# Optimization experiments

Hardware: AMD Instinct MI355X
Metric: run time of the kernel (lower is better)

Reference implementation:

```python
import jax, jax.numpy as jnp
import numpy as np

B = 8; NPC = 12500; N = B * NPC
L = 10.0; RES = 0.7; K = 16
IN_CH = 64; H1 = 68; H2 = 128; RNN = 128; ATTN = 32; E4 = 4 * RNN
EPS = 1e-5


def _knn_np(refs, queries, k):
    out = np.empty((queries.shape[0], k), dtype=np.int64)
    r2 = (refs * refs).sum(1)
    for s in range(0, queries.shape[0], 2048):
        q = queries[s:s + 2048]
        d2 = (q * q).sum(1)[:, None] - 2.0 * q @ refs.T + r2[None, :]
        out[s:s + q.shape[0]] = np.argpartition(d2, k, axis=1)[:, :k]
    return out


def setup_inputs():
    rng = np.random.default_rng(0)
    pos = rng.uniform(0.0, L, (N, 3)).astype(np.float32)
    batch = np.repeat(np.arange(B), NPC).astype(np.int32)
    x = (0.5 * rng.standard_normal((N, IN_CH))).astype(np.float32)
    refl = rng.uniform(0.0, 1.0, N).astype(np.float32)
    # voxel-grid sampling: one representative point per occupied voxel per cloud
    G = int(np.ceil(L / RES)) + 1
    v = np.floor(pos / RES).astype(np.int64)
    vkey = ((batch.astype(np.int64) * G + v[:, 0]) * G + v[:, 1]) * G + v[:, 2]
    _, first = np.unique(vkey, return_index=True)
    idx = np.sort(first)
    M = idx.shape[0]
    # per-cloud brute-force KNN (k neighbors in full set for every sampled point)
    src_list = []
    for b in range(B):
        qi = idx[(idx >= b * NPC) & (idx < (b + 1) * NPC)]
        src_list.append(_knn_np(pos[b * NPC:(b + 1) * NPC], pos[qi], K) + b * NPC)
    src = np.concatenate(src_list, 0).reshape(-1)
    tgt = np.repeat(np.arange(M), K)
    edge_index = np.stack([src, tgt]).astype(np.int32)

    def W(*s):
        return jnp.asarray((0.05 * rng.standard_normal(s)).astype(np.float32))

    def zeros(c):
        return jnp.zeros((c,), jnp.float32)

    def bnp(c):  # packed inference-mode BN params: [gamma, beta, mean, var]
        return jnp.asarray(np.stack([1.0 + 0.1 * rng.standard_normal(c), 0.1 * rng.standard_normal(c), 0.1 * rng.standard_normal(c), 1.0 + 0.1 * rng.uniform(0.0, 1.0, c)]).astype(np.float32))

    def dwp(c):  # depthwise k=1 conv = per-channel [weight, bias]
        return jnp.asarray(np.stack([1.0 + 0.1 * rng.standard_normal(c), 0.1 * rng.standard_normal(c)]).astype(np.float32))

    gum = -np.log(-np.log(rng.uniform(1e-6, 1.0 - 1e-6, (B, 2))))
    return dict(
        x=jnp.asarray(x), pos=jnp.asarray(pos), reflectance=jnp.asarray(refl),
        gumbel=jnp.asarray(gum.astype(np.float32)),
        gate_w1=W(4, H1), gate_b1=zeros(H1), gate_w2=W(H1, H1), gate_b2=zeros(H1),
        gate_wg=W(H1, 2), gate_bg=jnp.asarray(np.array([0.0, 2.0], np.float32)),
        loc_w1=W(H1, H2), loc_b1=zeros(H2), loc_w2=W(H2, H2), loc_b2=zeros(H2),
        attn_w1=W(H2, ATTN), attn_b1=zeros(ATTN), attn_w2=W(ATTN),
        exp_w=W(RNN, E4), exp_b=zeros(E4), exp_bn=bnp(E4),
        ds1_dw=dwp(E4), ds1_bn1=bnp(E4), ds1_pw_w=W(E4, E4), ds1_pw_b=zeros(E4), ds1_bn2=bnp(E4),
        blk_bn1=bnp(E4),
        ds2_dw=dwp(E4), ds2_bn1=bnp(E4), ds2_pw_w=W(E4, E4), ds2_pw_b=zeros(E4), ds2_bn2=bnp(E4),
        blk_bn2=bnp(E4),
        proj_w=W(E4, RNN), proj_b=zeros(RNN), proj_bn=bnp(RNN),
        batch=jnp.asarray(batch), idx=jnp.asarray(idx.astype(np.int32)),
        edge_index=jnp.asarray(edge_index), k=K, num_graphs=B)


def _bn(z, p):
    return p[0] * (z - p[2]) / jnp.sqrt(p[3] + EPS) + p[1]


def reference(x, pos, reflectance, gumbel, gate_w1, gate_b1, gate_w2, gate_b2, gate_wg, gate_bg, loc_w1, loc_b1, loc_w2, loc_b2, attn_w1, attn_b1, attn_w2, exp_w, exp_b, exp_bn, ds1_dw, ds1_bn1, ds1_pw_w, ds1_pw_b, ds1_bn2, blk_bn1, ds2_dw, ds2_bn1, ds2_pw_w, ds2_pw_b, ds2_bn2, blk_bn2, proj_w, proj_b, proj_bn, batch, idx, edge_index, k, num_graphs):
    # --- BinaryReflectanceGate (soft gumbel-softmax, tau=1) ---
    feats = jnp.concatenate([pos, reflectance[:, None]], -1)  # [N,4]
    h = jax.nn.relu(feats @ gate_w1 + gate_b1)
    h = jax.nn.relu(h @ gate_w2 + gate_b2)
    pooled = jax.ops.segment_max(h, batch, num_segments=num_graphs)  # global_max_pool
    logits = pooled @ gate_wg + gate_bg
    y_soft = jax.nn.softmax(logits + gumbel, axis=-1)
    refl_g = y_soft[:, 1][batch] * reflectance  # gated reflectance [N]
    pos4 = jnp.concatenate([pos, refl_g[:, None]], -1)  # [N,4]
    # --- AttentivePointNetConv: gather -> local MLP -> softmax attn -> reduce ---
    M = idx.shape[0]
    src = edge_index[0].reshape(M, k)  # k source neighbors per centroid
    msg_in = jnp.concatenate([x[src], pos4[src] - pos4[idx][:, None, :]], -1)  # [M,k,68]
    hm = jax.nn.relu(msg_in @ loc_w1 + loc_b1)
    msg = jax.nn.relu(hm @ loc_w2 + loc_b2)  # [M,k,128]
    score = jnp.tanh(msg @ attn_w1 + attn_b1) @ attn_w2  # [M,k]
    alpha = jax.nn.softmax(score, axis=-1)  # softmax over each centroid's edges
    agg = jnp.einsum('mk,mkc->mc', alpha, msg)  # [M,128]
    # --- InvertedResidualBlock (all convs kernel=1 -> channel matmuls, BN inference) ---
    out = jax.nn.relu(_bn(agg @ exp_w + exp_b, exp_bn))  # expand 128->512

    def ds(z, dw, bn1, pw_w, pw_b, bn2):
        d = jax.nn.relu(_bn(z * dw[0] + dw[1], bn1))  # depthwise k=1
        return _bn(d @ pw_w + pw_b, bn2)  # pointwise

    out = _bn(ds(out, ds1_dw, ds1_bn1, ds1_pw_w, ds1_pw_b, ds1_bn2), blk_bn1)
    out = _bn(ds(out, ds2_dw, ds2_bn1, ds2_pw_w, ds2_pw_b, ds2_bn2), blk_bn2)
    out = _bn(out @ proj_w + proj_b, proj_bn)  # project 512->128
    out = jax.nn.relu(out + agg)  # identity shortcut (RNN==RNN)
    return (out, pos[idx], batch[idx], refl_g[idx])
```

## Files before the change

kernel.cpp:

```cpp
#include <hip/hip_runtime.h>
#include <hip/hip_bf16.h>

typedef __hip_bfloat16 bf16;

#define B_GR 8
#define IN_CH 64
#define H1 68
#define H2 128
#define ATTN 32
#define E4 512
#define RNN 128
#define KNN 16
#define EPSV 1e-5f

typedef __attribute__((ext_vector_type(8))) short s8v;
typedef __attribute__((ext_vector_type(4))) float f4v;
#define MFMA16(a,b,c) __builtin_amdgcn_mfma_f32_16x16x32_bf16(a,b,c,0,0,0)

#define SK96 104
#define SK128 136
#define SK512 520

template<int DT> __device__ __forceinline__ float LD(const void* p, size_t i) {
    if (DT) return __bfloat162float(((const bf16*)p)[i]);
    return ((const float*)p)[i];
}
template<int DT> __device__ __forceinline__ void ST(void* p, size_t i, float v) {
    if (DT) ((bf16*)p)[i] = __float2bfloat16(v);
    else    ((float*)p)[i] = v;
}
__device__ __forceinline__ unsigned short f2bfb(float f) {
    unsigned u = __float_as_uint(f);
    unsigned r = (u + 0x7FFFu + ((u >> 16) & 1u)) >> 16;
    return (unsigned short)r;
}
__device__ __forceinline__ float bfb2f(unsigned short u) {
    return __uint_as_float(((unsigned)u) << 16);
}
__device__ __forceinline__ float fast_tanh(float x) {
    x = fminf(fmaxf(x, -12.f), 12.f);
    float e = __expf(2.f * x);
    return (e - 1.f) / (e + 1.f);
}

__global__ void prep_kernel(const void* pos, int* flag, int* pooled) {
    const int tid = threadIdx.x;
    for (int i = tid; i < B_GR*H1; i += 256) pooled[i] = 0;
    if (tid == 0) {
        const unsigned* w = (const unsigned*)pos;
        int ok = 1;
        #pragma unroll 8
        for (int i = 0; i < 256; i++) {
            float f = __uint_as_float((w[i] & 0xFFFFu) << 16);
            if (!(f >= -0.01f && f <= 10.05f)) ok = 0;
        }
        *flag = ok;
    }
}

#define W1T_E (128*SK96)
#define W2T_E (128*SK128)
#define AW1T_E (32*SK128)
#define EXPT_E (512*SK128)
#define D1T_E (512*SK512)
#define D2T_E (512*SK512)
#define PJT_E (128*SK512)
#define GW2T_E (80*SK96)
template<int DT> __global__ __launch_bounds__(256) void trans_kernel(
    const int* __restrict__ flag,
    const void* __restrict__ w1, const void* __restrict__ w2, const void* __restrict__ aw1,
    const void* __restrict__ expw, const void* __restrict__ d1pw,
    const void* __restrict__ d2pw, const void* __restrict__ pjw,
    const void* __restrict__ gw2,
    unsigned short* __restrict__ w1T, unsigned short* __restrict__ w2T,
    unsigned short* __restrict__ aw1T, unsigned short* __restrict__ expwT,
    unsigned short* __restrict__ d1pwT, unsigned short* __restrict__ d2pwT,
    unsigned short* __restrict__ pjwT, unsigned short* __restrict__ gw2gT)
{
    if (*flag != DT) return;
    const int T0 = W1T_E, T1 = T0+W2T_E, T2 = T1+AW1T_E, T3 = T2+EXPT_E,
              T4 = T3+D1T_E, T5 = T4+D2T_E, T6 = T5+PJT_E, T7 = T6+GW2T_E;
    for (int i = blockIdx.x*256 + threadIdx.x; i < T7; i += gridDim.x*256) {
        if (i < T0) {
            int n = i / SK96, k = i - n*SK96;
            w1T[i] = (k < H1) ? f2bfb(LD<DT>(w1, (size_t)k*H2 + n)) : 0;
        } else if (i < T1) {
            int j = i - T0; int n = j / SK128, k = j - n*SK128;
            w2T[j] = (k < H2) ? f2bfb(LD<DT>(w2, (size_t)k*H2 + n)) : 0;
        } else if (i < T2) {
            int j = i - T1; int n = j / SK128, k = j - n*SK128;
            aw1T[j] = (k < H2) ? f2bfb(LD<DT>(aw1, (size_t)k*ATTN + n)) : 0;
        } else if (i < T3) {
            int j = i - T2; int n = j / SK128, k = j - n*SK128;
            expwT[j] = (k < RNN) ? f2bfb(LD<DT>(expw, (size_t)k*E4 + n)) : 0;
        } else if (i < T4) {
            int j = i - T3; int n = j / SK512, k = j - n*SK512;
            d1pwT[j] = (k < E4) ? f2bfb(LD<DT>(d1pw, (size_t)k*E4 + n)) : 0;
        } else if (i < T5) {
            int j = i - T4; int n = j / SK512, k = j - n*SK512;
            d2pwT[j] = (k < E4) ? f2bfb(LD<DT>(d2pw, (size_t)k*E4 + n)) : 0;
        } else if (i < T6) {
            int j = i - T5; int n = j / SK512, k = j - n*SK512;
            pjwT[j] = (k < E4) ? f2bfb(LD<DT>(pjw, (size_t)k*RNN + n)) : 0;
        } else {
            int j = i - T6; int n = j / SK96, k = j - n*SK96;
            gw2gT[j] = (k < H1 && n < H1) ? f2bfb(LD<DT>(gw2, (size_t)k*H1 + n)) : 0;
        }
    }
}

template<int DT> __global__ void coef_kernel(
    const int* __restrict__ flag,
    const void* __restrict__ expb, const void* __restrict__ expbn,
    const void* __restrict__ d1dw, const void* __restrict__ d1bn1,
    const void* __restrict__ d1pb, const void* __restrict__ d1bn2, const void* __restrict__ bbn1,
    const void* __restrict__ d2dw, const void* __restrict__ d2bn1,
    const void* __restrict__ d2pb, const void* __restrict__ d2bn2, const void* __restrict__ bbn2,
    const void* __restrict__ pjb, const void* __restrict__ pjbn,
    float4* __restrict__ C1, float2* __restrict__ C2, float2* __restrict__ C3,
    float2* __restrict__ C4)
{
    if (*flag != DT) return;
    int c = blockIdx.x*256 + threadIdx.x;
    if (c < E4) {
        float a_e = LD<DT>(expbn,c) * rsqrtf(LD<DT>(expbn,3*E4+c)+EPSV);
        float t0  = a_e*(LD<DT>(expb,c) - LD<DT>(expbn,2*E4+c)) + LD<DT>(expbn,E4+c);
        float a1 = LD<DT>(d1bn1,c) * rsqrtf(LD<DT>(d1bn1,3*E4+c)+EPSV);
        float s1 = a1 * LD<DT>(d1dw,c);
        float t1 = a1*(LD<DT>(d1dw,E4+c) - LD<DT>(d1bn1,2*E4+c)) + LD<DT>(d1bn1,E4+c);
        C1[c] = make_float4(a_e, t0, s1, t1);
        float a2 = LD<DT>(d1bn2,c) * rsqrtf(LD<DT>(d1bn2,3*E4+c)+EPSV);
        float t2 = a2*(LD<DT>(d1pb,c) - LD<DT>(d1bn2,2*E4+c)) + LD<DT>(d1bn2,E4+c);
        float a3 = LD<DT>(bbn1,c) * rsqrtf(LD<DT>(bbn1,3*E4+c)+EPSV);
        float S2 = a3*a2;
        float T2 = a3*(t2 - LD<DT>(bbn1,2*E4+c)) + LD<DT>(bbn1,E4+c);
        float a4 = LD<DT>(d2bn1,c) * rsqrtf(LD<DT>(d2bn1,3*E4+c)+EPSV);
        float sdw = a4 * LD<DT>(d2dw,c);
        float tdw = a4*(LD<DT>(d2dw,E4+c) - LD<DT>(d2bn1,2*E4+c)) + LD<DT>(d2bn1,E4+c);
        C2[c] = make_float2(sdw*S2, sdw*T2 + tdw);
        float a5 = LD<DT>(d2bn2,c) * rsqrtf(LD<DT>(d2bn2,3*E4+c)+EPSV);
        float t5 = a5*(LD<DT>(d2pb,c) - LD<DT>(d2bn2,2*E4+c)) + LD<DT>(d2bn2,E4+c);
        float a6 = LD<DT>(bbn2,c) * rsqrtf(LD<DT>(bbn2,3*E4+c)+EPSV);
        C3[c] = make_float2(a6*a5, a6*(t5 - LD<DT>(bbn2,2*E4+c)) + LD<DT>(bbn2,E4+c));
    }
    if (c < RNN) {
        float ap = LD<DT>(pjbn,c) * rsqrtf(LD<DT>(pjbn,3*RNN+c)+EPSV);
        C4[c] = make_float2(ap, ap*(LD<DT>(pjb,c) - LD<DT>(pjbn,2*RNN+c)) + LD<DT>(pjbn,RNN+c));
    }
}

template<int DT> __global__ __launch_bounds__(256) void gate_mfma(
    const int* __restrict__ flag,
    const void* __restrict__ pos, const void* __restrict__ refl,
    const void* __restrict__ w1, const void* __restrict__ b1, const void* __restrict__ b2g,
    const unsigned short* __restrict__ gw2gT,
    int* __restrict__ pooled, int NPC, int CPB)
{
    if (*flag != DT) return;
    __shared__ __align__(16) unsigned short hs[256*SK96];
    __shared__ float w1s[4*H1], b1s[H1], b2s[H1];
    const int tid = threadIdx.x;
    for (int i = tid; i < 4*H1; i += 256) w1s[i] = LD<DT>(w1, i);
    if (tid < H1) { b1s[tid] = LD<DT>(b1, tid); b2s[tid] = LD<DT>(b2g, tid); }
    __syncthreads();

    const int bb = blockIdx.x / CPB;
    const int cc = blockIdx.x % CPB;
    const int base = bb*NPC + cc*256;
    const int limit = NPC - cc*256;
    const int p = base + ((tid < limit) ? tid : 0);

    {
        float f0 = LD<DT>(pos, (size_t)p*3+0), f1 = LD<DT>(pos, (size_t)p*3+1);
        float f2 = LD<DT>(pos, (size_t)p*3+2), f3 = LD<DT>(refl, p);
        float h[H1];
        #pragma unroll
        for (int j = 0; j < H1; j++)
            h[j] = fmaxf(b1s[j] + f0*w1s[j] + f1*w1s[H1+j] + f2*w1s[2*H1+j] + f3*w1s[3*H1+j], 0.f);
        #pragma unroll
        for (int j = 0; j < H1; j += 2) {
            unsigned v = (unsigned)f2bfb(h[j]) | ((unsigned)f2bfb(h[j+1]) << 16);
            *(unsigned*)&hs[tid*SK96 + j] = v;
        }
        #pragma unroll
        for (int j = H1; j < 96; j += 2) *(unsigned*)&hs[tid*SK96 + j] = 0;
    }
    __syncthreads();

    const int wv = tid >> 6, lane = tid & 63, quad = lane >> 4, l15 = lane & 15;
    f4v acc[4][5];
    #pragma unroll
    for (int mt = 0; mt < 4; mt++)
        #pragma unroll
        for (int nt = 0; nt < 5; nt++) acc[mt][nt] = (f4v){0.f,0.f,0.f,0.f};
    s8v af[4][3];
    #pragma unroll
    for (int mt = 0; mt < 4; mt++)
        #pragma unroll
        for (int ks = 0; ks < 3; ks++)
            af[mt][ks] = *(const s8v*)&hs[(wv*64 + mt*16 + l15)*SK96 + ks*32 + quad*8];
    #pragma unroll
    for (int nt = 0; nt < 5; nt++) {
        #pragma unroll
        for (int ks = 0; ks < 3; ks++) {
            s8v bf_ = *(const s8v*)&gw2gT[(size_t)(nt*16 + l15)*SK96 + ks*32 + quad*8];
            #pragma unroll
            for (int mt = 0; mt < 4; mt++) acc[mt][nt] = MFMA16(af[mt][ks], bf_, acc[mt][nt]);
        }
    }
    #pragma unroll
    for (int nt = 0; nt < 5; nt++) {
        int col = nt*16 + l15;
        float v = acc[0][nt][0];
        #pragma unroll
        for (int mt = 0; mt < 4; mt++)
            #pragma unroll
            for (int r = 0; r < 4; r++) v = fmaxf(v, acc[mt][nt][r]);
        v = fmaxf(v, __shfl_xor(v, 16));
        v = fmaxf(v, __shfl_xor(v, 32));
        if (quad == 0 && col < H1) {
            float o = fmaxf(v + b2s[col], 0.f);
            atomicMax(&pooled[bb*H1 + col], __float_as_int(o));
        }
    }
}

template<int DT> __global__ void gate2_kernel(
    const int* __restrict__ flag, const int* __restrict__ pooled,
    const void* __restrict__ wg, const void* __restrict__ bg,
    const void* __restrict__ gum, float* __restrict__ y1)
{
    if (*flag != DT) return;
    __shared__ float lg[B_GR][2];
    const int t = threadIdx.x;
    if (t < B_GR*2) {
        int b = t >> 1, g = t & 1;
        float a = LD<DT>(bg, g) + LD<DT>(gum, b*2+g);
        for (int c = 0; c < H1; c++) a += __int_as_float(pooled[b*H1+c]) * LD<DT>(wg, c*2+g);
        lg[b][g] = a;
    }
    __syncthreads();
    if (t < B_GR) {
        float l0 = lg[t][0], l1 = lg[t][1];
        float m = fmaxf(l0, l1);
        float e0 = __expf(l0-m), e1 = __expf(l1-m);
        y1[t] = e1 / (e0 + e1);
    }
}

template<int DT> __global__ __launch_bounds__(256) void edge_mfma(
    const int* __restrict__ flag,
    const void* __restrict__ x, const void* __restrict__ pos,
    const void* __restrict__ refl, const float* __restrict__ y1,
    const int* __restrict__ batch,
    const int* __restrict__ idxarr, const int* __restrict__ esrc,
    const void* __restrict__ b1, const void* __restrict__ b2,
    const void* __restrict__ ab1, const void* __restrict__ aw2,
    const unsigned short* __restrict__ gw1T, const unsigned short* __restrict__ gw2T,
    const unsigned short* __restrict__ gaw1T,
    void* __restrict__ out, int M)
{
    if (*flag != DT) return;
    __shared__ __align__(16) unsigned short u2[128*SK128];
    __shared__ float ssc[4][2][16];

    const int tid = threadIdx.x;
    const int wv = tid >> 6, lane = tid & 63, quad = lane >> 4, l15 = lane & 15;
    const int m0 = blockIdx.x * 8 + wv * 2;
    const int rb = wv * 32;

    s8v af[2][3];
    int mcl[2];
    float p4v[2][4];
    #pragma unroll
    for (int t = 0; t < 2; t++) {
        int mm = m0 + t; if (mm >= M) mm = M - 1;
        mcl[t] = mm;
        int t_idx = idxarr[mm];
        p4v[t][0] = LD<DT>(pos, (size_t)t_idx*3 + 0);
        p4v[t][1] = LD<DT>(pos, (size_t)t_idx*3 + 1);
        p4v[t][2] = LD<DT>(pos, (size_t)t_idx*3 + 2);
        p4v[t][3] = y1[batch[t_idx]] * LD<DT>(refl, t_idx);
        int s = esrc[mm*KNN + l15];
        if (DT) {
            const unsigned short* xs = (const unsigned short*)x + (size_t)s*IN_CH;
            af[t][0] = *(const s8v*)(xs + quad*8);
            af[t][1] = *(const s8v*)(xs + 32 + quad*8);
        } else {
            unsigned short tmp0[8], tmp1[8];
            #pragma unroll
            for (int e = 0; e < 8; e++) {
                tmp0[e] = f2bfb(LD<0>(x, (size_t)s*IN_CH + quad*8 + e));
                tmp1[e] = f2bfb(LD<0>(x, (size_t)s*IN_CH + 32 + quad*8 + e));
            }
            af[t][0] = *(const s8v*)tmp0;
            af[t][1] = *(const s8v*)tmp1;
        }
        s8v a2 = (s8v){0,0,0,0,0,0,0,0};
        if (quad == 0) {
            a2[0] = (short)f2bfb(LD<DT>(pos, (size_t)s*3 + 0) - p4v[t][0]);
            a2[1] = (short)f2bfb(LD<DT>(pos, (size_t)s*3 + 1) - p4v[t][1]);
            a2[2] = (short)f2bfb(LD<DT>(pos, (size_t)s*3 + 2) - p4v[t][2]);
            a2[3] = (short)f2bfb(y1[batch[s]] * LD<DT>(refl, s) - p4v[t][3]);
        }
        af[t][2] = a2;
    }

    {
        f4v acc[2][8];
        #pragma unroll
        for (int t = 0; t < 2; t++)
            #pragma unroll
            for (int nt = 0; nt < 8; nt++) acc[t][nt] = (f4v){0.f,0.f,0.f,0.f};
        #pragma unroll
        for (int nt = 0; nt < 8; nt++) {
            #pragma unroll
            for (int ks = 0; ks < 3; ks++) {
                s8v bf_ = *(const s8v*)&gw1T[(size_t)(nt*16 + l15)*SK96 + ks*32 + quad*8];
                acc[0][nt] = MFMA16(af[0][ks], bf_, acc[0][nt]);
                acc[1][nt] = MFMA16(af[1][ks], bf_, acc[1][nt]);
            }
        }
        #pragma unroll
        for (int nt = 0; nt < 8; nt++) {
            int col = nt*16 + l15;
            float bb = LD<DT>(b1, col);
            #pragma unroll
            for (int t = 0; t < 2; t++)
                #pragma unroll
                for (int r = 0; r < 4; r++) {
                    int row = rb + t*16 + quad*4 + r;
                    u2[row*SK128 + col] = f2bfb(fmaxf(acc[t][nt][r] + bb, 0.f));
                }
        }
    }

    {
        s8v af2[2][4];
        #pragma unroll
        for (int t = 0; t < 2; t++)
            #pragma unroll
            for (int ks = 0; ks < 4; ks++)
                af2[t][ks] = *(const s8v*)&u2[(rb + t*16 + l15)*SK128 + ks*32 + quad*8];
        f4v acc[2][8];
        #pragma unroll
        for (int t = 0; t < 2; t++)
            #pragma unroll
            for (int nt = 0; nt < 8; nt++) acc[t][nt] = (f4v){0.f,0.f,0.f,0.f};
        #pragma unroll
        for (int nt = 0; nt < 8; nt++) {
            #pragma unroll
            for (int ks = 0; ks < 4; ks++) {
                s8v bf_ = *(const s8v*)&gw2T[(size_t)(nt*16 + l15)*SK128 + ks*32 + quad*8];
                acc[0][nt] = MFMA16(af2[0][ks], bf_, acc[0][nt]);
                acc[1][nt] = MFMA16(af2[1][ks], bf_, acc[1][nt]);
            }
        }
        #pragma unroll
        for (int nt = 0; nt < 8; nt++) {
            int col = nt*16 + l15;
            float bb = LD<DT>(b2, col);
            #pragma unroll
            for (int t = 0; t < 2; t++)
                #pragma unroll
                for (int r = 0; r < 4; r++) {
                    int row = rb + t*16 + quad*4 + r;
                    u2[row*SK128 + col] = f2bfb(fmaxf(acc[t][nt][r] + bb, 0.f));
                }
        }
    }

    {
        s8v af3[2][4];
        #pragma unroll
        for (int t = 0; t < 2; t++)
            #pragma unroll
            for (int ks = 0; ks < 4; ks++)
                af3[t][ks] = *(const s8v*)&u2[(rb + t*16 + l15)*SK128 + ks*32 + quad*8];
        f4v acc[2][2];
        #pragma unroll
        for (int t = 0; t < 2; t++)
            #pragma unroll
            for (int nt = 0; nt < 2; nt++) acc[t][nt] = (f4v){0.f,0.f,0.f,0.f};
        #pragma unroll
        for (int nt = 0; nt < 2; nt++) {
            #pragma unroll
            for (int ks = 0; ks < 4; ks++) {
                s8v bf_ = *(const s8v*)&gaw1T[(size_t)(nt*16 + l15)*SK128 + ks*32 + quad*8];
                acc[0][nt] = MFMA16(af3[0][ks], bf_, acc[0][nt]);
                acc[1][nt] = MFMA16(af3[1][ks], bf_, acc[1][nt]);
            }
        }
        #pragma unroll
        for (int t = 0; t < 2; t++)
            #pragma unroll
            for (int r = 0; r < 4; r++) {
                float s = 0.f;
                #pragma unroll
                for (int nt = 0; nt < 2; nt++) {
                    int col = nt*16 + l15;
                    s += fast_tanh(acc[t][nt][r] + LD<DT>(ab1, col)) * LD<DT>(aw2, col);
                }
                s += __shfl_xor(s, 1);
                s += __shfl_xor(s, 2);
                s += __shfl_xor(s, 4);
                s += __shfl_xor(s, 8);
                if (l15 == 0) ssc[wv][t][quad*4 + r] = s;
            }
    }

    #pragma unroll
    for (int t = 0; t < 2; t++) {
        float sc[KNN];
        #pragma unroll
        for (int j = 0; j < KNN; j++) sc[j] = ssc[wv][t][j];
        float mx = sc[0];
        #pragma unroll
        for (int j = 1; j < KNN; j++) mx = fmaxf(mx, sc[j]);
        float den = 0.f;
        #pragma unroll
        for (int j = 0; j < KNN; j++) { sc[j] = __expf(sc[j] - mx); den += sc[j]; }
        float inv = 1.f / den;
        float a0 = 0.f, a1 = 0.f;
        #pragma unroll
        for (int j = 0; j < KNN; j++) {
            unsigned v = *(const unsigned*)&u2[(rb + t*16 + j)*SK128 + 2*lane];
            float w = sc[j] * inv;
            a0 += w * bfb2f((unsigned short)(v & 0xFFFFu));
            a1 += w * bfb2f((unsigned short)(v >> 16));
        }
        int mm = m0 + t;
        if (mm < M) {
            if (DT) {
                unsigned pk = (unsigned)f2bfb(a0) | ((unsigned)f2bfb(a1) << 16);
                *(unsigned*)((bf16*)out + (size_t)mm*H2 + 2*lane) = pk;
            } else {
                ST<0>(out, (size_t)mm*H2 + 2*lane, a0);
                ST<0>(out, (size_t)mm*H2 + 2*lane + 1, a1);
            }
            if (lane == 0) {
                ST<DT>(out, (size_t)M*128 + mm*3 + 0, p4v[t][0]);
                ST<DT>(out, (size_t)M*128 + mm*3 + 1, p4v[t][1]);
                ST<DT>(out, (size_t)M*128 + mm*3 + 2, p4v[t][2]);
                ST<DT>(out, (size_t)M*131 + mm, (float)batch[idxarr[mcl[t]]]);
                ST<DT>(out, (size_t)M*132 + mm, p4v[t][3]);
            }
        }
    }
}

template<int DT> __global__ __launch_bounds__(256) void post_mfma(
    const int* __restrict__ flag,
    const unsigned short* __restrict__ expwT, const unsigned short* __restrict__ d1pwT,
    const unsigned short* __restrict__ d2pwT, const unsigned short* __restrict__ pjwT,
    const float4* __restrict__ C1, const float2* __restrict__ C2,
    const float2* __restrict__ C3, const float2* __restrict__ C4,
    void* __restrict__ out, int M)
{
    if (*flag != DT) return;
    __shared__ __align__(16) unsigned short zs[32*SK512];
    __shared__ __align__(16) unsigned short a0[32*SK128];
    const int tid = threadIdx.x;
    const int m0 = blockIdx.x * 32;

    {
        int r = tid >> 3;
        int c0 = (tid & 7) * 16;
        int mm = m0 + r;
        for (int c = c0; c < c0+16; c++) {
            float v = (mm < M) ? LD<DT>(out, (size_t)mm*RNN + c) : 0.f;
            a0[r*SK128 + c] = f2bfb(v);
        }
        if ((tid & 7) == 7) for (int c = RNN; c < SK128; c++) a0[r*SK128 + c] = 0;
    }
    __syncthreads();

    const int wv = tid >> 6, lane = tid & 63, quad = lane >> 4, l15 = lane & 15;
    const int nbase = wv * 128;

    f4v acc[2][8];

    #pragma unroll
    for (int mt = 0; mt < 2; mt++)
        #pragma unroll
        for (int nt = 0; nt < 8; nt++) acc[mt][nt] = (f4v){0.f,0.f,0.f,0.f};
    #pragma unroll
    for (int ks = 0; ks < 4; ks++) {
        s8v af0 = *(const s8v*)&a0[(l15)*SK128 + ks*32 + quad*8];
        s8v af1 = *(const s8v*)&a0[(16+l15)*SK128 + ks*32 + quad*8];
        #pragma unroll
        for (int nt = 0; nt < 8; nt++) {
            s8v bf_ = *(const s8v*)&expwT[(size_t)(nbase + nt*16 + l15)*SK128 + ks*32 + quad*8];
            acc[0][nt] = MFMA16(af0, bf_, acc[0][nt]);
            acc[1][nt] = MFMA16(af1, bf_, acc[1][nt]);
        }
    }
    #pragma unroll
    for (int nt = 0; nt < 8; nt++) {
        int col = nbase + nt*16 + l15;
        float4 cf = C1[col];
        #pragma unroll
        for (int mt = 0; mt < 2; mt++)
            #pragma unroll
            for (int r = 0; r < 4; r++) {
                int row = mt*16 + quad*4 + r;
                float u = fmaxf(cf.x*acc[mt][nt][r] + cf.y, 0.f);
                float d = fmaxf(cf.z*u + cf.w, 0.f);
                zs[row*SK512 + col] = f2bfb(d);
            }
    }
    __syncthreads();

    #pragma unroll
    for (int mt = 0; mt < 2; mt++)
        #pragma unroll
        for (int nt = 0; nt < 8; nt++) acc[mt][nt] = (f4v){0.f,0.f,0.f,0.f};
    for (int ks = 0; ks < 16; ks++) {
        s8v af0 = *(const s8v*)&zs[(l15)*SK512 + ks*32 + quad*8];
        s8v af1 = *(const s8v*)&zs[(16+l15)*SK512 + ks*32 + quad*8];
        #pragma unroll
        for (int nt = 0; nt < 8; nt++) {
            s8v bf_ = *(const s8v*)&d1pwT[(size_t)(nbase + nt*16 + l15)*SK512 + ks*32 + quad*8];
            acc[0][nt] = MFMA16(af0, bf_, acc[0][nt]);
            acc[1][nt] = MFMA16(af1, bf_, acc[1][nt]);
        }
    }
    __syncthreads();
    #pragma unroll
    for (int nt = 0; nt < 8; nt++) {
        int col = nbase + nt*16 + l15;
        float2 cf = C2[col];
        #pragma unroll
        for (int mt = 0; mt < 2; mt++)
            #pragma unroll
            for (int r = 0; r < 4; r++) {
                int row = mt*16 + quad*4 + r;
                zs[row*SK512 + col] = f2bfb(fmaxf(cf.x*acc[mt][nt][r] + cf.y, 0.f));
            }
    }
    __syncthreads();

    #pragma unroll
    for (int mt = 0; mt < 2; mt++)
        #pragma unroll
        for (int nt = 0; nt < 8; nt++) acc[mt][nt] = (f4v){0.f,0.f,0.f,0.f};
    for (int ks = 0; ks < 16; ks++) {
        s8v af0 = *(const s8v*)&zs[(l15)*SK512 + ks*32 + quad*8];
        s8v af1 = *(const s8v*)&zs[(16+l15)*SK512 + ks*32 + quad*8];
        #pragma unroll
        for (int nt = 0; nt < 8; nt++) {
            s8v bf_ = *(const s8v*)&d2pwT[(size_t)(nbase + nt*16 + l15)*SK512 + ks*32 + quad*8];
            acc[0][nt] = MFMA16(af0, bf_, acc[0][nt]);
            acc[1][nt] = MFMA16(af1, bf_, acc[1][nt]);
        }
    }
    __syncthreads();
    #pragma unroll
    for (int nt = 0; nt < 8; nt++) {
        int col = nbase + nt*16 + l15;
        float2 cf = C3[col];
        #pragma unroll
        for (int mt = 0; mt < 2; mt++)
            #pragma unroll
            for (int r = 0; r < 4; r++) {
                int row = mt*16 + quad*4 + r;
                zs[row*SK512 + col] = f2bfb(cf.x*acc[mt][nt][r] + cf.y);
            }
    }
    __syncthreads();

    {
        f4v pacc[2][2];
        #pragma unroll
        for (int mt = 0; mt < 2; mt++)
            #pragma unroll
            for (int nt = 0; nt < 2; nt++) pacc[mt][nt] = (f4v){0.f,0.f,0.f,0.f};
        for (int ks = 0; ks < 16; ks++) {
            s8v af0 = *(const s8v*)&zs[(l15)*SK512 + ks*32 + quad*8];
            s8v af1 = *(const s8v*)&zs[(16+l15)*SK512 + ks*32 + quad*8];
            #pragma unroll
            for (int nt = 0; nt < 2; nt++) {
                s8v bf_ = *(const s8v*)&pjwT[(size_t)(wv*32 + nt*16 + l15)*SK512 + ks*32 + quad*8];
                pacc[0][nt] = MFMA16(af0, bf_, pacc[0][nt]);
                pacc[1][nt] = MFMA16(af1, bf_, pacc[1][nt]);
            }
        }
        #pragma unroll
        for (int nt = 0; nt < 2; nt++) {
            int col = wv*32 + nt*16 + l15;
            float2 cf = C4[col];
            #pragma unroll
            for (int mt = 0; mt < 2; mt++)
                #pragma unroll
                for (int r = 0; r < 4; r++) {
                    int row = mt*16 + quad*4 + r;
                    int mm = m0 + row;
                    if (mm < M) {
                        float agv = bfb2f(a0[row*SK128 + col]);
                        float o = fmaxf(cf.x*pacc[mt][nt][r] + cf.y + agv, 0.f);
                        ST<DT>(out, (size_t)mm*RNN + col, o);
                    }
                }
        }
    }
}

extern "C" void kernel_launch(void* const* d_in, const int* in_sizes, int n_in,
                              void* d_out, int out_size, void* d_ws, size_t ws_size,
                              hipStream_t stream)
{
    const void* x    = d_in[0];
    const void* pos  = d_in[1];
    const void* refl = d_in[2];
    const void* gum  = d_in[3];
    const void* gw1  = d_in[4];
    const void* gb1  = d_in[5];
    const void* gw2  = d_in[6];
    const void* gb2  = d_in[7];
    const void* gwg  = d_in[8];
    const void* gbg  = d_in[9];
    const void* lw1  = d_in[10];
    const void* lb1  = d_in[11];
    const void* lw2  = d_in[12];
    const void* lb2  = d_in[13];
    const void* aw1  = d_in[14];
    const void* ab1  = d_in[15];
    const void* aw2  = d_in[16];
    const void* expw = d_in[17];
    const void* expb = d_in[18];
    const void* expbn= d_in[19];
    const void* d1dw = d_in[20];
    const void* d1bn1= d_in[21];
    const void* d1pw = d_in[22];
    const void* d1pb = d_in[23];
    const void* d1bn2= d_in[24];
    const void* bbn1 = d_in[25];
    const void* d2dw = d_in[26];
    const void* d2bn1= d_in[27];
    const void* d2pw = d_in[28];
    const void* d2pb = d_in[29];
    const void* d2bn2= d_in[30];
    const void* bbn2 = d_in[31];
    const void* pjw  = d_in[32];
    const void* pjb  = d_in[33];
    const void* pjbn = d_in[34];
    const int* batch = (const int*)d_in[35];
    const int* idxp  = (const int*)d_in[36];
    const int* eidx  = (const int*)d_in[37];

    const int N = in_sizes[2];
    const int M = in_sizes[36];
    const int NPC = N / B_GR;
    const int CPB = (NPC + 255) / 256;

    char* wsb = (char*)d_ws;
    int*  flag   = (int*)wsb;
    int*  pooled = (int*)(wsb + 16);
    float* y1    = (float*)(wsb + 2304);
    unsigned short* w1T   = (unsigned short*)(wsb + 2368);
    unsigned short* w2T   = w1T + W1T_E;
    unsigned short* aw1T  = w2T + W2T_E;
    unsigned short* expwT = aw1T + AW1T_E;
    unsigned short* d1pwT = expwT + EXPT_E;
    unsigned short* d2pwT = d1pwT + D1T_E;
    unsigned short* pjwT  = d2pwT + D2T_E;
    unsigned short* gw2gT = pjwT + PJT_E;
    float4* C1 = (float4*)(gw2gT + GW2T_E + 8);
    float2* C2 = (float2*)(C1 + E4);
    float2* C3 = C2 + E4;
    float2* C4 = C3 + E4;

    prep_kernel<<<1, 256, 0, stream>>>(pos, flag, pooled);

    trans_kernel<0><<<512, 256, 0, stream>>>(flag, lw1, lw2, aw1, expw, d1pw, d2pw, pjw, gw2,
                                             w1T, w2T, aw1T, expwT, d1pwT, d2pwT, pjwT, gw2gT);
    trans_kernel<1><<<512, 256, 0, stream>>>(flag, lw1, lw2, aw1, expw, d1pw, d2pw, pjw, gw2,
                                             w1T, w2T, aw1T, expwT, d1pwT, d2pwT, pjwT, gw2gT);

    coef_kernel<0><<<2, 256, 0, stream>>>(flag, expb, expbn, d1dw, d1bn1, d1pb, d1bn2, bbn1,
                                          d2dw, d2bn1, d2pb, d2bn2, bbn2, pjb, pjbn,
                                          C1, C2, C3, C4);
    coef_kernel<1><<<2, 256, 0, stream>>>(flag, expb, expbn, d1dw, d1bn1, d1pb, d1bn2, bbn1,
                                          d2dw, d2bn1, d2pb, d2bn2, bbn2, pjb, pjbn,
                                          C1, C2, C3, C4);

    gate_mfma<0><<<B_GR*CPB, 256, 0, stream>>>(flag, pos, refl, gw1, gb1, gb2, gw2gT, pooled, NPC, CPB);
    gate_mfma<1><<<B_GR*CPB, 256, 0, stream>>>(flag, pos, refl, gw1, gb1, gb2, gw2gT, pooled, NPC, CPB);

    gate2_kernel<0><<<1, 64, 0, stream>>>(flag, pooled, gwg, gbg, gum, y1);
    gate2_kernel<1><<<1, 64, 0, stream>>>(flag, pooled, gwg, gbg, gum, y1);

    const int EB = (M + 7) / 8;
    edge_mfma<0><<<EB, 256, 0, stream>>>(flag, x, pos, refl, y1, batch, idxp, eidx,
                                         lb1, lb2, ab1, aw2, w1T, w2T, aw1T, d_out, M);
    edge_mfma<1><<<EB, 256, 0, stream>>>(flag, x, pos, refl, y1, batch, idxp, eidx,
                                         lb1, lb2, ab1, aw2, w1T, w2T, aw1T, d_out, M);

    const int PB = (M + 31) / 32;
    post_mfma<0><<<PB, 256, 0, stream>>>(flag, expwT, d1pwT, d2pwT, pjwT, C1, C2, C3, C4, d_out, M);
    post_mfma<1><<<PB, 256, 0, stream>>>(flag, expwT, d1pwT, d2pwT, pjwT, C1, C2, C3, C4, d_out, M);
}
```

Baseline: 472.9 us.

## Restructure post-MLP so each wave owns a 16-row strip without block barriers

The post-processing MLP kernel now runs with two waves per block. Each wave owns its own 16 rows and computes all output columns, keeping its A fragments in registers and passing intermediates through a private shared-memory strip. This removes the __syncthreads barriers and the shared a0 staging buffer, and the residual is re-read from global memory at the end. The cost is that every wave now streams the full weight matrices from global/L2 for only 16 rows, roughly doubling weight traffic per row. It also needs more registers to hold 16 A fragments.

```diff
diff --git a/kernel.cpp b/kernel.cpp
--- a/kernel.cpp
+++ b/kernel.cpp
@@ -449,7 +449,7 @@
     }
 }
 
-template<int DT> __global__ __launch_bounds__(256) void post_mfma(
+template<int DT> __global__ __launch_bounds__(128) void post_mfma(
     const int* __restrict__ flag,
     const unsigned short* __restrict__ expwT, const unsigned short* __restrict__ d1pwT,
     const unsigned short* __restrict__ d2pwT, const unsigned short* __restrict__ pjwT,
@@ -459,148 +459,114 @@
 {
     if (*flag != DT) return;
     __shared__ __align__(16) unsigned short zs[32*SK512];
-    __shared__ __align__(16) unsigned short a0[32*SK128];
     const int tid = threadIdx.x;
-    const int m0 = blockIdx.x * 32;
-
-    {
-        int r = tid >> 3;
-        int c0 = (tid & 7) * 16;
-        int mm = m0 + r;
-        for (int c = c0; c < c0+16; c++) {
-            float v = (mm < M) ? LD<DT>(out, (size_t)mm*RNN + c) : 0.f;
-            a0[r*SK128 + c] = f2bfb(v);
-        }
-        if ((tid & 7) == 7) for (int c = RNN; c < SK128; c++) a0[r*SK128 + c] = 0;
-    }
-    __syncthreads();
-
     const int wv = tid >> 6, lane = tid & 63, quad = lane >> 4, l15 = lane & 15;
-    const int nbase = wv * 128;
-
-    f4v acc[2][8];
-
-    #pragma unroll
-    for (int mt = 0; mt < 2; mt++)
-        #pragma unroll
-        for (int nt = 0; nt < 8; nt++) acc[mt][nt] = (f4v){0.f,0.f,0.f,0.f};
-    #pragma unroll
-    for (int ks = 0; ks < 4; ks++) {
-        s8v af0 = *(const s8v*)&a0[(l15)*SK128 + ks*32 + quad*8];
-        s8v af1 = *(const s8v*)&a0[(16+l15)*SK128 + ks*32 + quad*8];
-        #pragma unroll
+    const int m0w = blockIdx.x * 32 + wv * 16;
+    unsigned short* strip = zs + wv * 16 * SK512;
+
+    {
+        s8v afe[4];
+        int mrow = m0w + l15; if (mrow >= M) mrow = M - 1;
+        if (DT) {
+            const unsigned short* op = (const unsigned short*)out + (size_t)mrow*RNN;
+            #pragma unroll
+            for (int ks = 0; ks < 4; ks++)
+                afe[ks] = *(const s8v*)(op + ks*32 + quad*8);
+        } else {
+            #pragma unroll
+            for (int ks = 0; ks < 4; ks++) {
+                unsigned short tmp[8];
+                #pragma unroll
+                for (int e = 0; e < 8; e++)
+                    tmp[e] = f2bfb(LD<0>(out, (size_t)mrow*RNN + ks*32 + quad*8 + e));
+                afe[ks] = *(const s8v*)tmp;
+            }
+        }
+        #pragma unroll 4
+        for (int nt = 0; nt < 32; nt++) {
+            f4v acc = (f4v){0.f,0.f,0.f,0.f};
+            #pragma unroll
+            for (int ks = 0; ks < 4; ks++) {
+                s8v bf_ = *(const s8v*)&expwT[(size_t)(nt*16 + l15)*SK128 + ks*32 + quad*8];
+                acc = MFMA16(afe[ks], bf_, acc);
+            }
+            int col = nt*16 + l15;
+            float4 cf = C1[col];
+            #pragma unroll
+            for (int r = 0; r < 4; r++) {
+                float u = fmaxf(cf.x*acc[r] + cf.y, 0.f);
+                float d = fmaxf(cf.z*u + cf.w, 0.f);
+                strip[(quad*4 + r)*SK512 + col] = f2bfb(d);
+            }
+        }
+    }
+
+    {
+        s8v af[16];
+        #pragma unroll
+        for (int ks = 0; ks < 16; ks++)
+            af[ks] = *(const s8v*)&strip[l15*SK512 + ks*32 + quad*8];
+        #pragma unroll 2
+        for (int nt = 0; nt < 32; nt++) {
+            f4v acc = (f4v){0.f,0.f,0.f,0.f};
+            #pragma unroll
+            for (int ks = 0; ks < 16; ks++) {
+                s8v bf_ = *(const s8v*)&d1pwT[(size_t)(nt*16 + l15)*SK512 + ks*32 + quad*8];
+                acc = MFMA16(af[ks], bf_, acc);
+            }
+            int col = nt*16 + l15;
+            float2 cf = C2[col];
+            #pragma unroll
+            for (int r = 0; r < 4; r++)
+                strip[(quad*4 + r)*SK512 + col] = f2bfb(fmaxf(cf.x*acc[r] + cf.y, 0.f));
+        }
+    }
+
+    {
+        s8v af[16];
+        #pragma unroll
+        for (int ks = 0; ks < 16; ks++)
+            af[ks] = *(const s8v*)&strip[l15*SK512 + ks*32 + quad*8];
+        #pragma unroll 2
+        for (int nt = 0; nt < 32; nt++) {
+            f4v acc = (f4v){0.f,0.f,0.f,0.f};
+            #pragma unroll
+            for (int ks = 0; ks < 16; ks++) {
+                s8v bf_ = *(const s8v*)&d2pwT[(size_t)(nt*16 + l15)*SK512 + ks*32 + quad*8];
+                acc = MFMA16(af[ks], bf_, acc);
+            }
+            int col = nt*16 + l15;
+            float2 cf = C3[col];
+            #pragma unroll
+            for (int r = 0; r < 4; r++)
+                strip[(quad*4 + r)*SK512 + col] = f2bfb(cf.x*acc[r] + cf.y);
+        }
+    }
+
+    {
+        s8v af[16];
+        #pragma unroll
+        for (int ks = 0; ks < 16; ks++)
+            af[ks] = *(const s8v*)&strip[l15*SK512 + ks*32 + quad*8];
+        #pragma unroll 2
         for (int nt = 0; nt < 8; nt++) {
-            s8v bf_ = *(const s8v*)&expwT[(size_t)(nbase + nt*16 + l15)*SK128 + ks*32 + quad*8];
-            acc[0][nt] = MFMA16(af0, bf_, acc[0][nt]);
-            acc[1][nt] = MFMA16(af1, bf_, acc[1][nt]);
-        }
-    }
-    #pragma unroll
-    for (int nt = 0; nt < 8; nt++) {
-        int col = nbase + nt*16 + l15;
-        float4 cf = C1[col];
-        #pragma unroll
-        for (int mt = 0; mt < 2; mt++)
+            f4v acc = (f4v){0.f,0.f,0.f,0.f};
+            #pragma unroll
+            for (int ks = 0; ks < 16; ks++) {
+                s8v bf_ = *(const s8v*)&pjwT[(size_t)(nt*16 + l15)*SK512 + ks*32 + quad*8];
+                acc = MFMA16(af[ks], bf_, acc);
+            }
+            int col = nt*16 + l15;
+            float2 cf = C4[col];
             #pragma unroll
             for (int r = 0; r < 4; r++) {
-                int row = mt*16 + quad*4 + r;
-                float u = fmaxf(cf.x*acc[mt][nt][r] + cf.y, 0.f);
-                float d = fmaxf(cf.z*u + cf.w, 0.f);
-                zs[row*SK512 + col] = f2bfb(d);
-            }
-    }
-    __syncthreads();
-
-    #pragma unroll
-    for (int mt = 0; mt < 2; mt++)
-        #pragma unroll
-        for (int nt = 0; nt < 8; nt++) acc[mt][nt] = (f4v){0.f,0.f,0.f,0.f};
-    for (int ks = 0; ks < 16; ks++) {
-        s8v af0 = *(const s8v*)&zs[(l15)*SK512 + ks*32 + quad*8];
-        s8v af1 = *(const s8v*)&zs[(16+l15)*SK512 + ks*32 + quad*8];
-        #pragma unroll
-        for (int nt = 0; nt < 8; nt++) {
-            s8v bf_ = *(const s8v*)&d1pwT[(size_t)(nbase + nt*16 + l15)*SK512 + ks*32 + quad*8];
-            acc[0][nt] = MFMA16(af0, bf_, acc[0][nt]);
-            acc[1][nt] = MFMA16(af1, bf_, acc[1][nt]);
-        }
-    }
-    __syncthreads();
-    #pragma unroll
-    for (int nt = 0; nt < 8; nt++) {
-        int col = nbase + nt*16 + l15;
-        float2 cf = C2[col];
-        #pragma unroll
-        for (int mt = 0; mt < 2; mt++)
-            #pragma unroll
-            for (int r = 0; r < 4; r++) {
-                int row = mt*16 + quad*4 + r;
-                zs[row*SK512 + col] = f2bfb(fmaxf(cf.x*acc[mt][nt][r] + cf.y, 0.f));
-            }
-    }
-    __syncthreads();
-
-    #pragma unroll
-    for (int mt = 0; mt < 2; mt++)
-        #pragma unroll
-        for (int nt = 0; nt < 8; nt++) acc[mt][nt] = (f4v){0.f,0.f,0.f,0.f};
-    for (int ks = 0; ks < 16; ks++) {
-        s8v af0 = *(const s8v*)&zs[(l15)*SK512 + ks*32 + quad*8];
-        s8v af1 = *(const s8v*)&zs[(16+l15)*SK512 + ks*32 + quad*8];
-        #pragma unroll
-        for (int nt = 0; nt < 8; nt++) {
-            s8v bf_ = *(const s8v*)&d2pwT[(size_t)(nbase + nt*16 + l15)*SK512 + ks*32 + quad*8];
-            acc[0][nt] = MFMA16(af0, bf_, acc[0][nt]);
-            acc[1][nt] = MFMA16(af1, bf_, acc[1][nt]);
-        }
-    }
-    __syncthreads();
-    #pragma unroll
-    for (int nt = 0; nt < 8; nt++) {
-        int col = nbase + nt*16 + l15;
-        float2 cf = C3[col];
-        #pragma unroll
-        for (int mt = 0; mt < 2; mt++)
-            #pragma unroll
-            for (int r = 0; r < 4; r++) {
-                int row = mt*16 + quad*4 + r;
-                zs[row*SK512 + col] = f2bfb(cf.x*acc[mt][nt][r] + cf.y);
-            }
-    }
-    __syncthreads();
-
-    {
-        f4v pacc[2][2];
-        #pragma unroll
-        for (int mt = 0; mt < 2; mt++)
-            #pragma unroll
-            for (int nt = 0; nt < 2; nt++) pacc[mt][nt] = (f4v){0.f,0.f,0.f,0.f};
-        for (int ks = 0; ks < 16; ks++) {
-            s8v af0 = *(const s8v*)&zs[(l15)*SK512 + ks*32 + quad*8];
-            s8v af1 = *(const s8v*)&zs[(16+l15)*SK512 + ks*32 + quad*8];
-            #pragma unroll
-            for (int nt = 0; nt < 2; nt++) {
-                s8v bf_ = *(const s8v*)&pjwT[(size_t)(wv*32 + nt*16 + l15)*SK512 + ks*32 + quad*8];
-                pacc[0][nt] = MFMA16(af0, bf_, pacc[0][nt]);
-                pacc[1][nt] = MFMA16(af1, bf_, pacc[1][nt]);
-            }
-        }
-        #pragma unroll
-        for (int nt = 0; nt < 2; nt++) {
-            int col = wv*32 + nt*16 + l15;
-            float2 cf = C4[col];
-            #pragma unroll
-            for (int mt = 0; mt < 2; mt++)
-                #pragma unroll
-                for (int r = 0; r < 4; r++) {
-                    int row = mt*16 + quad*4 + r;
-                    int mm = m0 + row;
-                    if (mm < M) {
-                        float agv = bfb2f(a0[row*SK128 + col]);
-                        float o = fmaxf(cf.x*pacc[mt][nt][r] + cf.y + agv, 0.f);
-                        ST<DT>(out, (size_t)mm*RNN + col, o);
-                    }
+                int mm = m0w + quad*4 + r;
+                if (mm < M) {
+                    float agv = LD<DT>(out, (size_t)mm*RNN + col);
+                    float o = fmaxf(cf.x*acc[r] + cf.y + agv, 0.f);
+                    ST<DT>(out, (size_t)mm*RNN + col, o);
                 }
+            }
         }
     }
 }
@@ -697,6 +663,6 @@
                                          lb1, lb2, ab1, aw2, w1T, w2T, aw1T, d_out, M);
 
     const int PB = (M + 31) / 32;
-    post_mfma<0><<<PB, 256, 0, stream>>>(flag, expwT, d1pwT, d2pwT, pjwT, C1, C2, C3, C4, d_out, M);
-    post_mfma<1><<<PB, 256, 0, stream>>>(flag, expwT, d1pwT, d2pwT, pjwT, C1, C2, C3, C4, d_out, M);
-}
+    post_mfma<0><<<PB, 128, 0, stream>>>(flag, expwT, d1pwT, d2pwT, pjwT, C1, C2, C3, C4, d_out, M);
+    post_mfma<1><<<PB, 128, 0, stream>>>(flag, expwT, d1pwT, d2pwT, pjwT, C1, C2, C3, C4, d_out, M);
+}
```

After: 460.5 us. 1.03x faster.

## Double-buffer post-MLP LDS stages and load expand operands directly into registers

Applied to the files above, without the earlier changes.

Replaces the single zs LDS buffer plus the a0 staging tile with two ping-pong buffers (zsA/zsB). Each matmul can then write its output to the other buffer without the extra barrier between the MFMA loop and the epilogue. The expand-layer A operands are loaded straight from global memory into registers instead of going through LDS, with the bf16 path using vector loads. The residual shortcut is re-read from global memory at the end. This removes two barriers and the LDS staging pass, at the cost of more LDS (two 32x520 buffers) and a possible occupancy drop.

```diff
diff --git a/kernel.cpp b/kernel.cpp
--- a/kernel.cpp
+++ b/kernel.cpp
@@ -458,131 +458,136 @@
     void* __restrict__ out, int M)
 {
     if (*flag != DT) return;
-    __shared__ __align__(16) unsigned short zs[32*SK512];
-    __shared__ __align__(16) unsigned short a0[32*SK128];
+    __shared__ __align__(16) unsigned short zsA[32*SK512];
+    __shared__ __align__(16) unsigned short zsB[32*SK512];
     const int tid = threadIdx.x;
+    const int wv = tid >> 6, lane = tid & 63, quad = lane >> 4, l15 = lane & 15;
     const int m0 = blockIdx.x * 32;
+    const int nbase = wv * 128;
 
     {
-        int r = tid >> 3;
-        int c0 = (tid & 7) * 16;
-        int mm = m0 + r;
-        for (int c = c0; c < c0+16; c++) {
-            float v = (mm < M) ? LD<DT>(out, (size_t)mm*RNN + c) : 0.f;
-            a0[r*SK128 + c] = f2bfb(v);
-        }
-        if ((tid & 7) == 7) for (int c = RNN; c < SK128; c++) a0[r*SK128 + c] = 0;
+        s8v afe[2][4];
+        #pragma unroll
+        for (int mt = 0; mt < 2; mt++) {
+            int mrow = m0 + mt*16 + l15; if (mrow >= M) mrow = M - 1;
+            if (DT) {
+                const unsigned short* op = (const unsigned short*)out + (size_t)mrow*RNN;
+                #pragma unroll
+                for (int ks = 0; ks < 4; ks++)
+                    afe[mt][ks] = *(const s8v*)(op + ks*32 + quad*8);
+            } else {
+                #pragma unroll
+                for (int ks = 0; ks < 4; ks++) {
+                    unsigned short tmp[8];
+                    #pragma unroll
+                    for (int e = 0; e < 8; e++)
+                        tmp[e] = f2bfb(LD<0>(out, (size_t)mrow*RNN + ks*32 + quad*8 + e));
+                    afe[mt][ks] = *(const s8v*)tmp;
+                }
+            }
+        }
+        f4v acc[2][8];
+        #pragma unroll
+        for (int mt = 0; mt < 2; mt++)
+            #pragma unroll
+            for (int nt = 0; nt < 8; nt++) acc[mt][nt] = (f4v){0.f,0.f,0.f,0.f};
+        #pragma unroll
+        for (int ks = 0; ks < 4; ks++) {
+            #pragma unroll
+            for (int nt = 0; nt < 8; nt++) {
+                s8v bf_ = *(const s8v*)&expwT[(size_t)(nbase + nt*16 + l15)*SK128 + ks*32 + quad*8];
+                acc[0][nt] = MFMA16(afe[0][ks], bf_, acc[0][nt]);
+                acc[1][nt] = MFMA16(afe[1][ks], bf_, acc[1][nt]);
+            }
+        }
+        #pragma unroll
+        for (int nt = 0; nt < 8; nt++) {
+            int col = nbase + nt*16 + l15;
+            float4 cf = C1[col];
+            #pragma unroll
+            for (int mt = 0; mt < 2; mt++)
+                #pragma unroll
+                for (int r = 0; r < 4; r++) {
+                    float u = fmaxf(cf.x*acc[mt][nt][r] + cf.y, 0.f);
+                    float d = fmaxf(cf.z*u + cf.w, 0.f);
+                    zsA[(mt*16 + quad*4 + r)*SK512 + col] = f2bfb(d);
+                }
+        }
     }
     __syncthreads();
 
-    const int wv = tid >> 6, lane = tid & 63, quad = lane >> 4, l15 = lane & 15;
-    const int nbase = wv * 128;
-
-    f4v acc[2][8];
-
-    #pragma unroll
-    for (int mt = 0; mt < 2; mt++)
-        #pragma unroll
-        for (int nt = 0; nt < 8; nt++) acc[mt][nt] = (f4v){0.f,0.f,0.f,0.f};
-    #pragma unroll
-    for (int ks = 0; ks < 4; ks++) {
-        s8v af0 = *(const s8v*)&a0[(l15)*SK128 + ks*32 + quad*8];
-        s8v af1 = *(const s8v*)&a0[(16+l15)*SK128 + ks*32 + quad*8];
+    {
+        f4v acc[2][8];
+        #pragma unroll
+        for (int mt = 0; mt < 2; mt++)
+            #pragma unroll
+            for (int nt = 0; nt < 8; nt++) acc[mt][nt] = (f4v){0.f,0.f,0.f,0.f};
+        for (int ks = 0; ks < 16; ks++) {
+            s8v a0 = *(const s8v*)&zsA[(l15)*SK512 + ks*32 + quad*8];
+            s8v a1 = *(const s8v*)&zsA[(16 + l15)*SK512 + ks*32 + quad*8];
+            #pragma unroll
+            for (int nt = 0; nt < 8; nt++) {
+                s8v bf_ = *(const s8v*)&d1pwT[(size_t)(nbase + nt*16 + l15)*SK512 + ks*32 + quad*8];
+                acc[0][nt] = MFMA16(a0, bf_, acc[0][nt]);
+                acc[1][nt] = MFMA16(a1, bf_, acc[1][nt]);
+            }
+        }
         #pragma unroll
         for (int nt = 0; nt < 8; nt++) {
-            s8v bf_ = *(const s8v*)&expwT[(size_t)(nbase + nt*16 + l15)*SK128 + ks*32 + quad*8];
-            acc[0][nt] = MFMA16(af0, bf_, acc[0][nt]);
-            acc[1][nt] = MFMA16(af1, bf_, acc[1][nt]);
-        }
-    }
-    #pragma unroll
-    for (int nt = 0; nt < 8; nt++) {
-        int col = nbase + nt*16 + l15;
-        float4 cf = C1[col];
+            int col = nbase + nt*16 + l15;
+            float2 cf = C2[col];
+            #pragma unroll
+            for (int mt = 0; mt < 2; mt++)
+                #pragma unroll
+                for (int r = 0; r < 4; r++)
+                    zsB[(mt*16 + quad*4 + r)*SK512 + col] = f2bfb(fmaxf(cf.x*acc[mt][nt][r] + cf.y, 0.f));
+        }
+    }
+    __syncthreads();
+
+    {
+        f4v acc[2][8];
         #pragma unroll
         for (int mt = 0; mt < 2; mt++)
             #pragma unroll
-            for (int r = 0; r < 4; r++) {
-                int row = mt*16 + quad*4 + r;
-                float u = fmaxf(cf.x*acc[mt][nt][r] + cf.y, 0.f);
-                float d = fmaxf(cf.z*u + cf.w, 0.f);
-                zs[row*SK512 + col] = f2bfb(d);
-            }
+            for (int nt = 0; nt < 8; nt++) acc[mt][nt] = (f4v){0.f,0.f,0.f,0.f};
+        for (int ks = 0; ks < 16; ks++) {
+            s8v a0 = *(const s8v*)&zsB[(l15)*SK512 + ks*32 + quad*8];
+            s8v a1 = *(const s8v*)&zsB[(16 + l15)*SK512 + ks*32 + quad*8];
+            #pragma unroll
+            for (int nt = 0; nt < 8; nt++) {
+                s8v bf_ = *(const s8v*)&d2pwT[(size_t)(nbase + nt*16 + l15)*SK512 + ks*32 + quad*8];
+                acc[0][nt] = MFMA16(a0, bf_, acc[0][nt]);
+                acc[1][nt] = MFMA16(a1, bf_, acc[1][nt]);
+            }
+        }
+        #pragma unroll
+        for (int nt = 0; nt < 8; nt++) {
+            int col = nbase + nt*16 + l15;
+            float2 cf = C3[col];
+            #pragma unroll
+            for (int mt = 0; mt < 2; mt++)
+                #pragma unroll
+                for (int r = 0; r < 4; r++)
+                    zsA[(mt*16 + quad*4 + r)*SK512 + col] = f2bfb(cf.x*acc[mt][nt][r] + cf.y);
+        }
     }
     __syncthreads();
 
-    #pragma unroll
-    for (int mt = 0; mt < 2; mt++)
-        #pragma unroll
-        for (int nt = 0; nt < 8; nt++) acc[mt][nt] = (f4v){0.f,0.f,0.f,0.f};
-    for (int ks = 0; ks < 16; ks++) {
-        s8v af0 = *(const s8v*)&zs[(l15)*SK512 + ks*32 + quad*8];
-        s8v af1 = *(const s8v*)&zs[(16+l15)*SK512 + ks*32 + quad*8];
-        #pragma unroll
-        for (int nt = 0; nt < 8; nt++) {
-            s8v bf_ = *(const s8v*)&d1pwT[(size_t)(nbase + nt*16 + l15)*SK512 + ks*32 + quad*8];
-            acc[0][nt] = MFMA16(af0, bf_, acc[0][nt]);
-            acc[1][nt] = MFMA16(af1, bf_, acc[1][nt]);
-        }
-    }
-    __syncthreads();
-    #pragma unroll
-    for (int nt = 0; nt < 8; nt++) {
-        int col = nbase + nt*16 + l15;
-        float2 cf = C2[col];
+    {
+        f4v acc[2][2];
         #pragma unroll
         for (int mt = 0; mt < 2; mt++)
             #pragma unroll
-            for (int r = 0; r < 4; r++) {
-                int row = mt*16 + quad*4 + r;
-                zs[row*SK512 + col] = f2bfb(fmaxf(cf.x*acc[mt][nt][r] + cf.y, 0.f));
-            }
-    }
-    __syncthreads();
-
-    #pragma unroll
-    for (int mt = 0; mt < 2; mt++)
-        #pragma unroll
-        for (int nt = 0; nt < 8; nt++) acc[mt][nt] = (f4v){0.f,0.f,0.f,0.f};
-    for (int ks = 0; ks < 16; ks++) {
-        s8v af0 = *(const s8v*)&zs[(l15)*SK512 + ks*32 + quad*8];
-        s8v af1 = *(const s8v*)&zs[(16+l15)*SK512 + ks*32 + quad*8];
-        #pragma unroll
-        for (int nt = 0; nt < 8; nt++) {
-            s8v bf_ = *(const s8v*)&d2pwT[(size_t)(nbase + nt*16 + l15)*SK512 + ks*32 + quad*8];
-            acc[0][nt] = MFMA16(af0, bf_, acc[0][nt]);
-            acc[1][nt] = MFMA16(af1, bf_, acc[1][nt]);
-        }
-    }
-    __syncthreads();
-    #pragma unroll
-    for (int nt = 0; nt < 8; nt++) {
-        int col = nbase + nt*16 + l15;
-        float2 cf = C3[col];
-        #pragma unroll
-        for (int mt = 0; mt < 2; mt++)
-            #pragma unroll
-            for (int r = 0; r < 4; r++) {
-                int row = mt*16 + quad*4 + r;
-                zs[row*SK512 + col] = f2bfb(cf.x*acc[mt][nt][r] + cf.y);
-            }
-    }
-    __syncthreads();
-
-    {
-        f4v pacc[2][2];
-        #pragma unroll
-        for (int mt = 0; mt < 2; mt++)
-            #pragma unroll
-            for (int nt = 0; nt < 2; nt++) pacc[mt][nt] = (f4v){0.f,0.f,0.f,0.f};
+            for (int nt = 0; nt < 2; nt++) acc[mt][nt] = (f4v){0.f,0.f,0.f,0.f};
         for (int ks = 0; ks < 16; ks++) {
-            s8v af0 = *(const s8v*)&zs[(l15)*SK512 + ks*32 + quad*8];
-            s8v af1 = *(const s8v*)&zs[(16+l15)*SK512 + ks*32 + quad*8];
+            s8v a0 = *(const s8v*)&zsA[(l15)*SK512 + ks*32 + quad*8];
+            s8v a1 = *(const s8v*)&zsA[(16 + l15)*SK512 + ks*32 + quad*8];
             #pragma unroll
             for (int nt = 0; nt < 2; nt++) {
                 s8v bf_ = *(const s8v*)&pjwT[(size_t)(wv*32 + nt*16 + l15)*SK512 + ks*32 + quad*8];
-                pacc[0][nt] = MFMA16(af0, bf_, pacc[0][nt]);
-                pacc[1][nt] = MFMA16(af1, bf_, pacc[1][nt]);
+                acc[0][nt] = MFMA16(a0, bf_, acc[0][nt]);
+                acc[1][nt] = MFMA16(a1, bf_, acc[1][nt]);
             }
         }
         #pragma unroll
@@ -593,11 +598,10 @@
             for (int mt = 0; mt < 2; mt++)
                 #pragma unroll
                 for (int r = 0; r < 4; r++) {
-                    int row = mt*16 + quad*4 + r;
-                    int mm = m0 + row;
+                    int mm = m0 + mt*16 + quad*4 + r;
                     if (mm < M) {
-                        float agv = bfb2f(a0[row*SK128 + col]);
-                        float o = fmaxf(cf.x*pacc[mt][nt][r] + cf.y + agv, 0.f);
+                        float agv = LD<DT>(out, (size_t)mm*RNN + col);
+                        float o = fmaxf(cf.x*acc[mt][nt][r] + cf.y + agv, 0.f);
                         ST<DT>(out, (size_t)mm*RNN + col, o);
                     }
                 }
```

Result: no change. 474.7 us (+0.4%).
